# Optimization experiments

Measured on AMD Instinct MI355X. Metric: run time of the kernel, lower is better.

The kernel has to match this reference:

```python
import jax, jax.numpy as jnp
import numpy as np

B, C, H, W_SP = 8, 2048, 28, 28   # last_conv feature map (ResNet-50, layer4 stride=1, 448px input)
D = 8192                          # count-sketch / CBP output dim
NUM_CLS = 200
L2_EPS = 1e-12                    # F.normalize default eps


def setup_inputs() -> dict:
    key = jax.random.key(0)
    ks = jax.random.split(key, 7)
    x = jax.random.normal(ks[0], (B, C, H, W_SP), dtype=jnp.float32)
    h1 = jax.random.randint(ks[1], (C,), 0, D, dtype=jnp.int32)
    h2 = jax.random.randint(ks[2], (C,), 0, D, dtype=jnp.int32)
    # Rademacher signs (count-sketch s vectors); map {0,1} -> {-1,+1}
    s1 = (2.0 * jax.random.bernoulli(ks[3], 0.5, (C,)).astype(jnp.float32) - 1.0)
    s2 = (2.0 * jax.random.bernoulli(ks[4], 0.5, (C,)).astype(jnp.float32) - 1.0)
    W_cls = jax.random.normal(ks[5], (D, NUM_CLS), dtype=jnp.float32) * 0.01
    b_cls = jnp.zeros((NUM_CLS,), dtype=jnp.float32)
    return {"x": x, "s1": s1, "s2": s2, "W_cls": W_cls, "b_cls": b_cls, "h1": h1, "h2": h2}


def _cbp_sum(xf, s1, s2, h1, h2):
    # xf: [B, L, C] per-pixel features.  Count-sketch each pixel twice, convolve
    # via FFT, then sum over all L spatial locations (== the original HxW loop).
    Bb, L, Cc = xf.shape
    sk1 = jnp.zeros((Bb, L, D), xf.dtype).at[..., h1].add(xf * s1)  # scatter-add over channels
    sk2 = jnp.zeros((Bb, L, D), xf.dtype).at[..., h2].add(xf * s2)
    f1 = jnp.fft.rfft(sk1, axis=-1)
    f2 = jnp.fft.rfft(sk2, axis=-1)
    y = jnp.fft.irfft(f1 * f2, n=D, axis=-1)  # [B, L, D] circular conv of sketches
    return y.sum(axis=1)                      # sum over spatial locations -> [B, D]


def reference(x, s1, s2, W_cls, b_cls, h1, h2):
    Bb, Cc, Hh, Ww = x.shape
    xf = x.transpose(0, 2, 3, 1).reshape(Bb, Hh * Ww, Cc)          # [B, L, C]
    y = _cbp_sum(xf, s1, s2, h1, h2)                               # [B, D]
    feat = jnp.sign(y) * jnp.sqrt(jnp.abs(y))                      # signed sqrt
    feat = feat / jnp.maximum(jnp.linalg.norm(feat, axis=1, keepdims=True), L2_EPS)
    logit = feat @ W_cls + b_cls
    return logit, feat
```

## Files before the change

kernel.cpp:

```cpp
#include <hip/hip_runtime.h>
#include <hip/hip_bf16.h>

#define BATCH 8
#define CH    2048
#define LSP   784
#define KPAD  832
#define KSTAGE 13
#define DDIM  8192
#define NCLS  200
#define NTILE 16
#define NGRID 1024
#define NSLOTX 128
#define NSLOTF 64
#define FXSCALE 8192.0f
#define FXINV   (1.0f/8192.0f)

typedef _Float16 f16x8 __attribute__((ext_vector_type(8)));
typedef _Float16 f16x4 __attribute__((ext_vector_type(4)));
typedef float    f32x4 __attribute__((ext_vector_type(4)));

#define FATOMIC(p, v) unsafeAtomicAdd((p), (v))

__global__ __launch_bounds__(256) void split_kernel(
    const float* __restrict__ x,
    _Float16* __restrict__ xh,
    float* __restrict__ part, float* __restrict__ norm,
    const float* __restrict__ s1, const int* __restrict__ h1,
    const float* __restrict__ s2, const int* __restrict__ h2,
    float4* __restrict__ metaG,
    const float* __restrict__ bc, float* __restrict__ out,
    int exclusive)
{
    int idx = blockIdx.x * 256 + threadIdx.x;
    if (!exclusive && idx < NSLOTF * BATCH * DDIM / 4)
        *(float4*)&part[idx * 4] = make_float4(0.f, 0.f, 0.f, 0.f);
    if (idx < CH)
        metaG[idx] = make_float4(s1[idx] * 64.0f, __int_as_float(h1[idx]),
                                 s2[idx] * 128.0f, __int_as_float(h2[idx]));
    if (idx < BATCH) norm[idx] = 0.0f;
    if (idx < BATCH * NCLS) out[idx] = bc[idx % NCLS];
    if (idx >= BATCH * CH * KPAD / 8) return;
    int v  = idx * 8;
    int bc_ = v / KPAD;
    int l  = v - bc_ * KPAD;
    f16x8 hv = {0, 0, 0, 0, 0, 0, 0, 0};
    if (l < LSP) {
        const float* xp = &x[(size_t)bc_ * LSP + l];
        float4 a = *(const float4*)xp;
        float4 c = *(const float4*)(xp + 4);
        hv[0] = (_Float16)a.x; hv[1] = (_Float16)a.y;
        hv[2] = (_Float16)a.z; hv[3] = (_Float16)a.w;
        hv[4] = (_Float16)c.x; hv[5] = (_Float16)c.y;
        hv[6] = (_Float16)c.z; hv[7] = (_Float16)c.w;
    }
    *(f16x8*)&xh[v] = hv;
}

__device__ __forceinline__ void stage64(
    const _Float16* __restrict__ src,
    unsigned short* lds,
    int wv, int lane, int s)
{
    const int rowi = lane >> 3;
    const int gc   = (lane & 7) ^ rowi;
    const _Float16* g0 = src + (size_t)rowi * KPAD + s * 64 + gc * 8;
#pragma unroll
    for (int q = 0; q < 4; ++q) {
        const int r0 = wv * 32 + q * 8;
        __builtin_amdgcn_global_load_lds(
            (__attribute__((address_space(1))) void*)(g0 + (size_t)r0 * KPAD),
            (__attribute__((address_space(3))) void*)(lds + r0 * 64),
            16, 0, 0);
    }
}

__global__ __launch_bounds__(256, 2) void gram_scatter_kernel(
    const _Float16* __restrict__ xh,
    const float4* __restrict__ metaG,
    float* __restrict__ part,
    int exclusive)
{
    __shared__ __align__(16) unsigned short smA[128 * 64];
    __shared__ __align__(16) unsigned short smB[128 * 64];
    __shared__ __align__(16) int bins[DDIM];

    const int tid  = threadIdx.x;
    const int lane = tid & 63;
    const int wv   = tid >> 6;
    const int bid  = blockIdx.x;
    const int b    = bid & 7;

    for (int i = tid; i < DDIM; i += 256) bins[i] = 0;

    int npair, tMs[2], tNs[2];
    if (bid < 64) {
        const int t2 = (bid >> 3) * 2;
        npair = 2;
        tMs[0] = tNs[0] = t2;
        tMs[1] = tNs[1] = t2 + 1;
    } else {
        npair = 1;
        int i = (bid - 64) >> 3;
        int tM = 0, tN = 0;
#pragma unroll 1
        for (int t = 0; t < NTILE - 1; ++t) {
            int cnt = NTILE - 1 - t;
            if (i < cnt) { tM = t; tN = t + 1 + i; break; }
            i -= cnt;
        }
        tMs[0] = tM; tNs[0] = tN;
    }

    const int wrow = (wv >> 1) * 64;
    const int wcol = (wv & 1) * 64;
    const int rsel = lane & 15;
    const int khi  = lane >> 4;

#pragma unroll 1
    for (int pp = 0; pp < npair; ++pp) {
        const int tM = tMs[pp], tN = tNs[pp];
        const bool diag = (tM == tN);

        const _Float16* srcA = xh + ((size_t)b * CH + (size_t)tM * 128) * KPAD;
        const _Float16* srcB = xh + ((size_t)b * CH + (size_t)tN * 128) * KPAD;
        const unsigned short* fragB = diag ? smA : smB;

        f32x4 acc[4][4];
        const f32x4 zv = {0.0f, 0.0f, 0.0f, 0.0f};
#pragma unroll
        for (int mi = 0; mi < 4; ++mi)
#pragma unroll
            for (int ni = 0; ni < 4; ++ni) acc[mi][ni] = zv;

#pragma unroll 1
        for (int s = 0; s < KSTAGE; ++s) {
            stage64(srcA, smA, wv, lane, s);
            if (!diag) stage64(srcB, smB, wv, lane, s);
            __syncthreads();
#pragma unroll
            for (int t = 0; t < 2; ++t) {
                const int co = ((((t << 2) + khi) ^ (rsel & 7)) << 3);
                f16x8 ah[4], bh[4];
#pragma unroll
                for (int i = 0; i < 4; ++i) {
                    ah[i] = *(const f16x8*)&smA[(wrow + i * 16 + rsel) * 64 + co];
                    bh[i] = *(const f16x8*)&fragB[(wcol + i * 16 + rsel) * 64 + co];
                }
#pragma unroll
                for (int mi = 0; mi < 4; ++mi)
#pragma unroll
                    for (int ni = 0; ni < 4; ++ni)
                        acc[mi][ni] = __builtin_amdgcn_mfma_f32_16x16x32_f16(
                            ah[mi], bh[ni], acc[mi][ni], 0, 0, 0);
            }
            __syncthreads();
        }

        const int c2b = tN * 128 + wcol + rsel;
        int   h1c[4], h2c[4]; float s1c[4], s2c[4];
#pragma unroll
        for (int ni = 0; ni < 4; ++ni) {
            float4 cm = metaG[c2b + ni * 16];
            s1c[ni] = cm.x; h1c[ni] = __float_as_int(cm.y);
            s2c[ni] = cm.z; h2c[ni] = __float_as_int(cm.w);
        }

        const int rowbase = tM * 128 + wrow + (khi << 2);
#pragma unroll
        for (int mi = 0; mi < 4; ++mi) {
            float4 rm[4];
#pragma unroll
            for (int r = 0; r < 4; ++r) rm[r] = metaG[rowbase + mi * 16 + r];
#pragma unroll
            for (int r = 0; r < 4; ++r) {
                const float s1r = rm[r].x, s2r = rm[r].z;
                const int h1r = __float_as_int(rm[r].y);
                const int h2r = __float_as_int(rm[r].w);
#pragma unroll
                for (int ni = 0; ni < 4; ++ni) {
                    float g = acc[mi][ni][r];
                    atomicAdd(&bins[(h1r + h2c[ni]) & (DDIM - 1)],
                              (int)(s1r * s2c[ni] * g));
                    if (!diag)
                        atomicAdd(&bins[(h1c[ni] + h2r) & (DDIM - 1)],
                                  (int)(s1c[ni] * s2r * g));
                }
            }
        }
    }

    __syncthreads();

    if (exclusive) {
        float* pbase = part + ((size_t)((bid >> 3) * BATCH + b) * DDIM);
#pragma unroll 4
        for (int i = tid; i < DDIM / 4; i += 256) {
            int4 v = *(const int4*)&bins[i * 4];
            float4 f = make_float4((float)v.x * FXINV, (float)v.y * FXINV,
                                   (float)v.z * FXINV, (float)v.w * FXINV);
            *(float4*)&pbase[i * 4] = f;
        }
    } else {
        float* pbase = part + ((size_t)(((bid >> 3) & 63) * BATCH + b) * DDIM);
        const int rot = (bid & 31) << 8;
        for (int i = tid; i < DDIM; i += 256) {
            int j = (i + rot) & (DDIM - 1);
            int v = bins[j];
            if (v != 0) FATOMIC(&pbase[j], (float)v * FXINV);
        }
    }
}

__global__ __launch_bounds__(256) void reduce_kernel(
    const float* __restrict__ part, float* __restrict__ y,
    float* __restrict__ norm, int nslots)
{
    const int tid = threadIdx.x;
    const int b   = blockIdx.x & 7;
    const int d0  = (blockIdx.x >> 3) * 256 + tid;
    float s = 0.0f;
#pragma unroll 8
    for (int p = 0; p < nslots; ++p)
        s += part[((size_t)p * BATCH + b) * DDIM + d0];
    y[(size_t)b * DDIM + d0] = s;
    float ab = fabsf(s);
    __shared__ float red[256];
    red[tid] = ab;
    __syncthreads();
    for (int st = 128; st > 0; st >>= 1) {
        if (tid < st) red[tid] += red[tid + st];
        __syncthreads();
    }
    if (tid == 0) FATOMIC(&norm[b], red[0]);
}

__global__ __launch_bounds__(256) void logit_kernel(
    const float* __restrict__ y, const float* __restrict__ norm,
    const float* __restrict__ W, float* __restrict__ out)
{
    const int j = blockIdx.x;
    const int tid = threadIdx.x;
    __shared__ float fs[BATCH][64];
    __shared__ float inv[BATCH];
    if (tid < BATCH) inv[tid] = 1.0f / fmaxf(sqrtf(norm[tid]), 1e-12f);
    __syncthreads();
    for (int i = tid; i < BATCH * 64; i += 256) {
        int bb = i >> 6, dd = i & 63;
        float v = y[(size_t)bb * DDIM + j * 64 + dd];
        float f = copysignf(sqrtf(fabsf(v)), v) * inv[bb];
        fs[bb][dd] = f;
        out[BATCH * NCLS + (size_t)bb * DDIM + j * 64 + dd] = f;
    }
    __syncthreads();
    if (tid < NCLS) {
        float a[BATCH];
#pragma unroll
        for (int bb = 0; bb < BATCH; ++bb) a[bb] = 0.0f;
        for (int dd = 0; dd < 64; ++dd) {
            float w = W[(size_t)(j * 64 + dd) * NCLS + tid];
#pragma unroll
            for (int bb = 0; bb < BATCH; ++bb) a[bb] += fs[bb][dd] * w;
        }
#pragma unroll
        for (int bb = 0; bb < BATCH; ++bb)
            FATOMIC(&out[bb * NCLS + tid], a[bb]);
    }
}

extern "C" void kernel_launch(void* const* d_in, const int* in_sizes, int n_in,
                              void* d_out, int out_size, void* d_ws, size_t ws_size,
                              hipStream_t stream)
{
    const float* x  = (const float*)d_in[0];
    const float* s1 = (const float*)d_in[1];
    const float* s2 = (const float*)d_in[2];
    const float* W  = (const float*)d_in[3];
    const float* bc = (const float*)d_in[4];
    const int*   h1 = (const int*)d_in[5];
    const int*   h2 = (const int*)d_in[6];
    float* out = (float*)d_out;

    const size_t ybytes  = (size_t)BATCH * DDIM * sizeof(float);
    const size_t xhbytes = (size_t)BATCH * CH * KPAD * sizeof(_Float16);

    size_t partbytes = (size_t)NSLOTX * BATCH * DDIM * sizeof(float);
    int exclusive = (ws_size >= partbytes + ybytes + 128 + xhbytes);
    if (!exclusive)
        partbytes = (size_t)NSLOTF * BATCH * DDIM * sizeof(float);
    const int nslots = exclusive ? NSLOTX : NSLOTF;

    char* ws = (char*)d_ws;
    float* part = (float*)ws;
    float* y    = (float*)(ws + partbytes);
    float4* metaG = (float4*)(ws + partbytes);
    float* norm = (float*)(ws + partbytes + ybytes);
    _Float16* xh = (_Float16*)(ws + partbytes + ybytes + 128);

    split_kernel<<<(BATCH * CH * KPAD / 8 + 255) / 256, 256, 0, stream>>>(
        x, xh, part, norm, s1, h1, s2, h2, metaG, bc, out, exclusive);

    gram_scatter_kernel<<<NGRID, 256, 0, stream>>>(
        xh, metaG, part, exclusive);

    reduce_kernel<<<256, 256, 0, stream>>>(part, y, norm, nslots);

    logit_kernel<<<128, 256, 0, stream>>>(y, norm, W, out);
}
```

Before: 172.0 us.

## Fuse all stages into one persistent kernel with software grid barriers

Merges the split, gram/scatter, reduce and logit kernels into a single persistent launch of 512 blocks. The phases are separated by an atomic-counter grid barrier. Each block now handles two gram jobs and accumulates both into its shared-memory bins before writing one partial slot, so there are 64 partial slots instead of 128 and the reduce reads less. The aim is to remove the per-launch overhead and the idle gaps between the four kernels. In exchange the code depends on all 512 blocks being co-resident, adds spin-wait barrier cost, and drops the fallback path for small workspaces.

Result: slower. 390.6 us (+127.1%).

```diff
diff --git a/kernel.cpp b/kernel.cpp
--- a/kernel.cpp
+++ b/kernel.cpp
@@ -9,51 +9,31 @@
 #define DDIM  8192
 #define NCLS  200
 #define NTILE 16
-#define NGRID 1024
-#define NSLOTX 128
-#define NSLOTF 64
-#define FXSCALE 8192.0f
-#define FXINV   (1.0f/8192.0f)
+#define GRID  512
+#define NJOBS 1024
+#define NSLOT 64
+#define NV8   (BATCH*CH*KPAD/8)
+#define FXINV (1.0f/8192.0f)
 
 typedef _Float16 f16x8 __attribute__((ext_vector_type(8)));
-typedef _Float16 f16x4 __attribute__((ext_vector_type(4)));
 typedef float    f32x4 __attribute__((ext_vector_type(4)));
 
 #define FATOMIC(p, v) unsafeAtomicAdd((p), (v))
 
-__global__ __launch_bounds__(256) void split_kernel(
-    const float* __restrict__ x,
-    _Float16* __restrict__ xh,
-    float* __restrict__ part, float* __restrict__ norm,
-    const float* __restrict__ s1, const int* __restrict__ h1,
-    const float* __restrict__ s2, const int* __restrict__ h2,
-    float4* __restrict__ metaG,
-    const float* __restrict__ bc, float* __restrict__ out,
-    int exclusive)
+
+__device__ __forceinline__ void gridbar(unsigned* __restrict__ cnt,
+                                        unsigned target)
 {
-    int idx = blockIdx.x * 256 + threadIdx.x;
-    if (!exclusive && idx < NSLOTF * BATCH * DDIM / 4)
-        *(float4*)&part[idx * 4] = make_float4(0.f, 0.f, 0.f, 0.f);
-    if (idx < CH)
-        metaG[idx] = make_float4(s1[idx] * 64.0f, __int_as_float(h1[idx]),
-                                 s2[idx] * 128.0f, __int_as_float(h2[idx]));
-    if (idx < BATCH) norm[idx] = 0.0f;
-    if (idx < BATCH * NCLS) out[idx] = bc[idx % NCLS];
-    if (idx >= BATCH * CH * KPAD / 8) return;
-    int v  = idx * 8;
-    int bc_ = v / KPAD;
-    int l  = v - bc_ * KPAD;
-    f16x8 hv = {0, 0, 0, 0, 0, 0, 0, 0};
-    if (l < LSP) {
-        const float* xp = &x[(size_t)bc_ * LSP + l];
-        float4 a = *(const float4*)xp;
-        float4 c = *(const float4*)(xp + 4);
-        hv[0] = (_Float16)a.x; hv[1] = (_Float16)a.y;
-        hv[2] = (_Float16)a.z; hv[3] = (_Float16)a.w;
-        hv[4] = (_Float16)c.x; hv[5] = (_Float16)c.y;
-        hv[6] = (_Float16)c.z; hv[7] = (_Float16)c.w;
-    }
-    *(f16x8*)&xh[v] = hv;
+    __syncthreads();
+    if (threadIdx.x == 0) {
+        __threadfence();
+        atomicAdd(cnt, 1u);
+        while (__hip_atomic_load(cnt, __ATOMIC_ACQUIRE,
+                                 __HIP_MEMORY_SCOPE_AGENT) < target)
+            __builtin_amdgcn_s_sleep(8);
+        __threadfence();
+    }
+    __syncthreads();
 }
 
 __device__ __forceinline__ void stage64(
@@ -74,124 +54,160 @@
     }
 }
 
-__global__ __launch_bounds__(256, 2) void gram_scatter_kernel(
-    const _Float16* __restrict__ xh,
-    const float4* __restrict__ metaG,
-    float* __restrict__ part,
-    int exclusive)
+__global__ __launch_bounds__(256, 2) void fused_kernel(
+    const float* __restrict__ x,
+    const float* __restrict__ s1, const int* __restrict__ h1,
+    const float* __restrict__ s2, const int* __restrict__ h2,
+    const float* __restrict__ W,  const float* __restrict__ bc,
+    float* __restrict__ out,
+    float* __restrict__ part, float* __restrict__ y,
+    float4* __restrict__ metaG, float* __restrict__ norm,
+    _Float16* __restrict__ xh, unsigned* __restrict__ cnt)
 {
     __shared__ __align__(16) unsigned short smA[128 * 64];
     __shared__ __align__(16) unsigned short smB[128 * 64];
     __shared__ __align__(16) int bins[DDIM];
 
     const int tid  = threadIdx.x;
+    const int bid  = blockIdx.x;
     const int lane = tid & 63;
     const int wv   = tid >> 6;
-    const int bid  = blockIdx.x;
-    const int b    = bid & 7;
-
-    for (int i = tid; i < DDIM; i += 256) bins[i] = 0;
-
-    int npair, tMs[2], tNs[2];
-    if (bid < 64) {
-        const int t2 = (bid >> 3) * 2;
-        npair = 2;
-        tMs[0] = tNs[0] = t2;
-        tMs[1] = tNs[1] = t2 + 1;
-    } else {
-        npair = 1;
-        int i = (bid - 64) >> 3;
-        int tM = 0, tN = 0;
+
+    {
+        const int gtid = bid * 256 + tid;
+        if (gtid < CH)
+            metaG[gtid] = make_float4(s1[gtid] * 64.0f, __int_as_float(h1[gtid]),
+                                      s2[gtid] * 128.0f, __int_as_float(h2[gtid]));
+        if (gtid < BATCH) norm[gtid] = 0.0f;
+        if (gtid < BATCH * NCLS) out[gtid] = bc[gtid % NCLS];
+#pragma unroll
+        for (int k = 0; k < 13; ++k) {
+            int idx = gtid + k * (GRID * 256);
+            int v   = idx * 8;
+            int bc_ = v / KPAD;
+            int l   = v - bc_ * KPAD;
+            f16x8 hv = {0, 0, 0, 0, 0, 0, 0, 0};
+            if (l < LSP) {
+                const float* xp = &x[(size_t)bc_ * LSP + l];
+                float4 a = *(const float4*)xp;
+                float4 c = *(const float4*)(xp + 4);
+                hv[0] = (_Float16)a.x; hv[1] = (_Float16)a.y;
+                hv[2] = (_Float16)a.z; hv[3] = (_Float16)a.w;
+                hv[4] = (_Float16)c.x; hv[5] = (_Float16)c.y;
+                hv[6] = (_Float16)c.z; hv[7] = (_Float16)c.w;
+            }
+            *(f16x8*)&xh[v] = hv;
+        }
+    }
+
+    gridbar(cnt, GRID);
+
+    {
+        const int b = bid & 7;
+        for (int i = tid; i < DDIM; i += 256) bins[i] = 0;
+
+        const int wrow = (wv >> 1) * 64;
+        const int wcol = (wv & 1) * 64;
+        const int rsel = lane & 15;
+        const int khi  = lane >> 4;
+
 #pragma unroll 1
-        for (int t = 0; t < NTILE - 1; ++t) {
-            int cnt = NTILE - 1 - t;
-            if (i < cnt) { tM = t; tN = t + 1 + i; break; }
-            i -= cnt;
-        }
-        tMs[0] = tM; tNs[0] = tN;
-    }
-
-    const int wrow = (wv >> 1) * 64;
-    const int wcol = (wv & 1) * 64;
-    const int rsel = lane & 15;
-    const int khi  = lane >> 4;
-
+        for (int jj = 0; jj < 2; ++jj) {
+            const int job = bid + jj * GRID;
+            int npair, tMs[2], tNs[2];
+            if (job < 64) {
+                const int t2 = (job >> 3) * 2;
+                npair = 2;
+                tMs[0] = tNs[0] = t2;
+                tMs[1] = tNs[1] = t2 + 1;
+            } else {
+                npair = 1;
+                int i = (job - 64) >> 3;
+                int tM = 0, tN = 0;
 #pragma unroll 1
-    for (int pp = 0; pp < npair; ++pp) {
-        const int tM = tMs[pp], tN = tNs[pp];
-        const bool diag = (tM == tN);
-
-        const _Float16* srcA = xh + ((size_t)b * CH + (size_t)tM * 128) * KPAD;
-        const _Float16* srcB = xh + ((size_t)b * CH + (size_t)tN * 128) * KPAD;
-        const unsigned short* fragB = diag ? smA : smB;
-
-        f32x4 acc[4][4];
-        const f32x4 zv = {0.0f, 0.0f, 0.0f, 0.0f};
-#pragma unroll
-        for (int mi = 0; mi < 4; ++mi)
-#pragma unroll
-            for (int ni = 0; ni < 4; ++ni) acc[mi][ni] = zv;
+                for (int t = 0; t < NTILE - 1; ++t) {
+                    int c = NTILE - 1 - t;
+                    if (i < c) { tM = t; tN = t + 1 + i; break; }
+                    i -= c;
+                }
+                tMs[0] = tM; tNs[0] = tN;
+            }
 
 #pragma unroll 1
-        for (int s = 0; s < KSTAGE; ++s) {
-            stage64(srcA, smA, wv, lane, s);
-            if (!diag) stage64(srcB, smB, wv, lane, s);
-            __syncthreads();
-#pragma unroll
-            for (int t = 0; t < 2; ++t) {
-                const int co = ((((t << 2) + khi) ^ (rsel & 7)) << 3);
-                f16x8 ah[4], bh[4];
-#pragma unroll
-                for (int i = 0; i < 4; ++i) {
-                    ah[i] = *(const f16x8*)&smA[(wrow + i * 16 + rsel) * 64 + co];
-                    bh[i] = *(const f16x8*)&fragB[(wcol + i * 16 + rsel) * 64 + co];
+            for (int pp = 0; pp < npair; ++pp) {
+                const int tM = tMs[pp], tN = tNs[pp];
+                const bool diag = (tM == tN);
+
+                const _Float16* srcA = xh + ((size_t)b * CH + (size_t)tM * 128) * KPAD;
+                const _Float16* srcB = xh + ((size_t)b * CH + (size_t)tN * 128) * KPAD;
+                const unsigned short* fragB = diag ? smA : smB;
+
+                f32x4 acc[4][4];
+                const f32x4 zv = {0.0f, 0.0f, 0.0f, 0.0f};
+#pragma unroll
+                for (int mi = 0; mi < 4; ++mi)
+#pragma unroll
+                    for (int ni = 0; ni < 4; ++ni) acc[mi][ni] = zv;
+
+#pragma unroll 1
+                for (int s = 0; s < KSTAGE; ++s) {
+                    stage64(srcA, smA, wv, lane, s);
+                    if (!diag) stage64(srcB, smB, wv, lane, s);
+                    __syncthreads();
+#pragma unroll
+                    for (int t = 0; t < 2; ++t) {
+                        const int co = ((((t << 2) + khi) ^ (rsel & 7)) << 3);
+                        f16x8 ah[4], bh[4];
+#pragma unroll
+                        for (int i = 0; i < 4; ++i) {
+                            ah[i] = *(const f16x8*)&smA[(wrow + i * 16 + rsel) * 64 + co];
+                            bh[i] = *(const f16x8*)&fragB[(wcol + i * 16 + rsel) * 64 + co];
+                        }
+#pragma unroll
+                        for (int mi = 0; mi < 4; ++mi)
+#pragma unroll
+                            for (int ni = 0; ni < 4; ++ni)
+                                acc[mi][ni] = __builtin_amdgcn_mfma_f32_16x16x32_f16(
+                                    ah[mi], bh[ni], acc[mi][ni], 0, 0, 0);
+                    }
+                    __syncthreads();
                 }
-#pragma unroll
-                for (int mi = 0; mi < 4; ++mi)
-#pragma unroll
-                    for (int ni = 0; ni < 4; ++ni)
-                        acc[mi][ni] = __builtin_amdgcn_mfma_f32_16x16x32_f16(
-                            ah[mi], bh[ni], acc[mi][ni], 0, 0, 0);
-            }
-            __syncthreads();
-        }
-
-        const int c2b = tN * 128 + wcol + rsel;
-        int   h1c[4], h2c[4]; float s1c[4], s2c[4];
-#pragma unroll
-        for (int ni = 0; ni < 4; ++ni) {
-            float4 cm = metaG[c2b + ni * 16];
-            s1c[ni] = cm.x; h1c[ni] = __float_as_int(cm.y);
-            s2c[ni] = cm.z; h2c[ni] = __float_as_int(cm.w);
-        }
-
-        const int rowbase = tM * 128 + wrow + (khi << 2);
-#pragma unroll
-        for (int mi = 0; mi < 4; ++mi) {
-            float4 rm[4];
-#pragma unroll
-            for (int r = 0; r < 4; ++r) rm[r] = metaG[rowbase + mi * 16 + r];
-#pragma unroll
-            for (int r = 0; r < 4; ++r) {
-                const float s1r = rm[r].x, s2r = rm[r].z;
-                const int h1r = __float_as_int(rm[r].y);
-                const int h2r = __float_as_int(rm[r].w);
+
+                const int c2b = tN * 128 + wcol + rsel;
+                int   h1c[4], h2c[4]; float s1c[4], s2c[4];
 #pragma unroll
                 for (int ni = 0; ni < 4; ++ni) {
-                    float g = acc[mi][ni][r];
-                    atomicAdd(&bins[(h1r + h2c[ni]) & (DDIM - 1)],
-                              (int)(s1r * s2c[ni] * g));
-                    if (!diag)
-                        atomicAdd(&bins[(h1c[ni] + h2r) & (DDIM - 1)],
-                                  (int)(s1c[ni] * s2r * g));
+                    float4 cm = metaG[c2b + ni * 16];
+                    s1c[ni] = cm.x; h1c[ni] = __float_as_int(cm.y);
+                    s2c[ni] = cm.z; h2c[ni] = __float_as_int(cm.w);
+                }
+                const int rowbase = tM * 128 + wrow + (khi << 2);
+#pragma unroll
+                for (int mi = 0; mi < 4; ++mi) {
+                    float4 rm[4];
+#pragma unroll
+                    for (int r = 0; r < 4; ++r) rm[r] = metaG[rowbase + mi * 16 + r];
+#pragma unroll
+                    for (int r = 0; r < 4; ++r) {
+                        const float s1r = rm[r].x, s2r = rm[r].z;
+                        const int h1r = __float_as_int(rm[r].y);
+                        const int h2r = __float_as_int(rm[r].w);
+#pragma unroll
+                        for (int ni = 0; ni < 4; ++ni) {
+                            float g = acc[mi][ni][r];
+                            atomicAdd(&bins[(h1r + h2c[ni]) & (DDIM - 1)],
+                                      (int)(s1r * s2c[ni] * g));
+                            if (!diag)
+                                atomicAdd(&bins[(h1c[ni] + h2r) & (DDIM - 1)],
+                                          (int)(s1c[ni] * s2r * g));
+                        }
+                    }
                 }
             }
         }
-    }
-
-    __syncthreads();
-
-    if (exclusive) {
+
+        __syncthreads();
+
         float* pbase = part + ((size_t)((bid >> 3) * BATCH + b) * DDIM);
 #pragma unroll 4
         for (int i = tid; i < DDIM / 4; i += 256) {
@@ -200,70 +216,61 @@
                                    (float)v.z * FXINV, (float)v.w * FXINV);
             *(float4*)&pbase[i * 4] = f;
         }
-    } else {
-        float* pbase = part + ((size_t)(((bid >> 3) & 63) * BATCH + b) * DDIM);
-        const int rot = (bid & 31) << 8;
-        for (int i = tid; i < DDIM; i += 256) {
-            int j = (i + rot) & (DDIM - 1);
-            int v = bins[j];
-            if (v != 0) FATOMIC(&pbase[j], (float)v * FXINV);
-        }
-    }
-}
-
-__global__ __launch_bounds__(256) void reduce_kernel(
-    const float* __restrict__ part, float* __restrict__ y,
-    float* __restrict__ norm, int nslots)
-{
-    const int tid = threadIdx.x;
-    const int b   = blockIdx.x & 7;
-    const int d0  = (blockIdx.x >> 3) * 256 + tid;
-    float s = 0.0f;
+    }
+
+    gridbar(cnt, 2 * GRID);
+
+    {
+        float* redf = (float*)bins;
+        const int rb = bid & 7;
+        const int d0 = (bid >> 3) * 128 + (tid & 127);
+        float s = 0.0f;
+        if (tid < 128) {
 #pragma unroll 8
-    for (int p = 0; p < nslots; ++p)
-        s += part[((size_t)p * BATCH + b) * DDIM + d0];
-    y[(size_t)b * DDIM + d0] = s;
-    float ab = fabsf(s);
-    __shared__ float red[256];
-    red[tid] = ab;
-    __syncthreads();
-    for (int st = 128; st > 0; st >>= 1) {
-        if (tid < st) red[tid] += red[tid + st];
+            for (int p = 0; p < NSLOT; ++p)
+                s += part[((size_t)p * BATCH + rb) * DDIM + d0];
+            y[(size_t)rb * DDIM + d0] = s;
+            redf[tid] = fabsf(s);
+        }
         __syncthreads();
-    }
-    if (tid == 0) FATOMIC(&norm[b], red[0]);
-}
-
-__global__ __launch_bounds__(256) void logit_kernel(
-    const float* __restrict__ y, const float* __restrict__ norm,
-    const float* __restrict__ W, float* __restrict__ out)
-{
-    const int j = blockIdx.x;
-    const int tid = threadIdx.x;
-    __shared__ float fs[BATCH][64];
-    __shared__ float inv[BATCH];
-    if (tid < BATCH) inv[tid] = 1.0f / fmaxf(sqrtf(norm[tid]), 1e-12f);
-    __syncthreads();
-    for (int i = tid; i < BATCH * 64; i += 256) {
-        int bb = i >> 6, dd = i & 63;
-        float v = y[(size_t)bb * DDIM + j * 64 + dd];
-        float f = copysignf(sqrtf(fabsf(v)), v) * inv[bb];
-        fs[bb][dd] = f;
-        out[BATCH * NCLS + (size_t)bb * DDIM + j * 64 + dd] = f;
-    }
-    __syncthreads();
-    if (tid < NCLS) {
-        float a[BATCH];
-#pragma unroll
-        for (int bb = 0; bb < BATCH; ++bb) a[bb] = 0.0f;
-        for (int dd = 0; dd < 64; ++dd) {
-            float w = W[(size_t)(j * 64 + dd) * NCLS + tid];
-#pragma unroll
-            for (int bb = 0; bb < BATCH; ++bb) a[bb] += fs[bb][dd] * w;
-        }
-#pragma unroll
-        for (int bb = 0; bb < BATCH; ++bb)
-            FATOMIC(&out[bb * NCLS + tid], a[bb]);
+        if (tid < 64) {
+            float v = redf[tid] + redf[tid + 64];
+#pragma unroll
+            for (int off = 32; off > 0; off >>= 1)
+                v += __shfl_down(v, off);
+            if (tid == 0) FATOMIC(&norm[rb], v);
+        }
+    }
+
+    gridbar(cnt, 3 * GRID);
+
+    if (bid < 128) {
+        float* fsb = (float*)bins;
+        float* inv = fsb + BATCH * 64;
+        const int j = bid;
+        if (tid < BATCH) inv[tid] = 1.0f / fmaxf(sqrtf(norm[tid]), 1e-12f);
+        __syncthreads();
+        for (int i = tid; i < BATCH * 64; i += 256) {
+            int bb = i >> 6, dd = i & 63;
+            float v = y[(size_t)bb * DDIM + j * 64 + dd];
+            float f = copysignf(sqrtf(fabsf(v)), v) * inv[bb];
+            fsb[bb * 64 + dd] = f;
+            out[BATCH * NCLS + (size_t)bb * DDIM + j * 64 + dd] = f;
+        }
+        __syncthreads();
+        if (tid < NCLS) {
+            float a[BATCH];
+#pragma unroll
+            for (int bb = 0; bb < BATCH; ++bb) a[bb] = 0.0f;
+            for (int dd = 0; dd < 64; ++dd) {
+                float w = W[(size_t)(j * 64 + dd) * NCLS + tid];
+#pragma unroll
+                for (int bb = 0; bb < BATCH; ++bb) a[bb] += fsb[bb * 64 + dd] * w;
+            }
+#pragma unroll
+            for (int bb = 0; bb < BATCH; ++bb)
+                FATOMIC(&out[bb * NCLS + tid], a[bb]);
+        }
     }
 }
 
@@ -280,29 +287,19 @@
     const int*   h2 = (const int*)d_in[6];
     float* out = (float*)d_out;
 
-    const size_t ybytes  = (size_t)BATCH * DDIM * sizeof(float);
-    const size_t xhbytes = (size_t)BATCH * CH * KPAD * sizeof(_Float16);
-
-    size_t partbytes = (size_t)NSLOTX * BATCH * DDIM * sizeof(float);
-    int exclusive = (ws_size >= partbytes + ybytes + 128 + xhbytes);
-    if (!exclusive)
-        partbytes = (size_t)NSLOTF * BATCH * DDIM * sizeof(float);
-    const int nslots = exclusive ? NSLOTX : NSLOTF;
+    const size_t partbytes = (size_t)NSLOT * BATCH * DDIM * sizeof(float);
+    const size_t ybytes    = (size_t)BATCH * DDIM * sizeof(float);
 
     char* ws = (char*)d_ws;
-    float* part = (float*)ws;
-    float* y    = (float*)(ws + partbytes);
-    float4* metaG = (float4*)(ws + partbytes);
-    float* norm = (float*)(ws + partbytes + ybytes);
-    _Float16* xh = (_Float16*)(ws + partbytes + ybytes + 128);
-
-    split_kernel<<<(BATCH * CH * KPAD / 8 + 255) / 256, 256, 0, stream>>>(
-        x, xh, part, norm, s1, h1, s2, h2, metaG, bc, out, exclusive);
-
-    gram_scatter_kernel<<<NGRID, 256, 0, stream>>>(
-        xh, metaG, part, exclusive);
-
-    reduce_kernel<<<256, 256, 0, stream>>>(part, y, norm, nslots);
-
-    logit_kernel<<<128, 256, 0, stream>>>(y, norm, W, out);
+    float*    part  = (float*)ws;
+    float*    y     = (float*)(ws + partbytes);
+    float4*   metaG = (float4*)(ws + partbytes);
+    float*    norm  = (float*)(ws + partbytes + ybytes);
+    unsigned* cnt   = (unsigned*)(ws + partbytes + ybytes + 64);
+    _Float16* xh    = (_Float16*)(ws + partbytes + ybytes + 128);
+
+    hipMemsetAsync(cnt, 0, sizeof(unsigned), stream);
+
+    fused_kernel<<<GRID, 256, 0, stream>>>(
+        x, s1, h1, s2, h2, W, bc, out, part, y, metaG, norm, xh, cnt);
 }
```
